# Kernel tuning notes

Hardware: AMD Instinct MI355X
Metric: run time of the kernel (lower is better)

The kernel has to match this reference:

```python
import jax, jax.numpy as jnp
import numpy as np

BETA = 0.25


def setup_inputs() -> dict:
    key = jax.random.key(0)
    k1, k2 = jax.random.split(key)
    inputs = jax.random.normal(k1, (32, 4096, 64), dtype=jnp.float32)
    # VarianceScaling(uniform) ~ small-magnitude init; plain normal scaled works for a numeric reference
    codebook = jax.random.normal(k2, (1024, 64), dtype=jnp.float32) * (1.0 / np.sqrt(64.0))
    return {"inputs": inputs, "codebook": codebook}


def reference(inputs, codebook):
    D = codebook.shape[-1]
    flat = jnp.reshape(inputs, (-1, D))                      # [N, D]
    flat_sqr = jnp.sum(flat ** 2, axis=-1, keepdims=True)    # [N, 1]
    code_sqr = jnp.sum(codebook ** 2, axis=-1)[None, :]      # [1, K]
    # full pairwise squared distances [N, K]
    distances = flat_sqr - 2.0 * (flat @ codebook.T) + code_sqr
    encoding_indices = jnp.reshape(jnp.argmin(distances, axis=-1), inputs.shape[:-1])
    quantize = codebook[encoding_indices]                    # gather -> [..., D]
    encoding_loss = jnp.mean((jax.lax.stop_gradient(inputs) - quantize) ** 2)
    commit_loss = jnp.mean((inputs - jax.lax.stop_gradient(quantize)) ** 2)
    loss = encoding_loss + BETA * commit_loss
    # straight-through estimator
    z_q = inputs + jax.lax.stop_gradient(quantize - inputs)
    return loss, z_q, encoding_indices
```

## Files before the change

kernel.cpp:

```cpp
#include <hip/hip_runtime.h>

#define N_ROWS 131072
#define D 64
#define K_CODES 1024

typedef _Float16 f16x8 __attribute__((ext_vector_type(8)));
typedef float    f32x4 __attribute__((ext_vector_type(4)));

#define MFMA16(a, b, c) __builtin_amdgcn_mfma_f32_16x16x32_f16((a), (b), (c), 0, 0, 0)

__global__ __launch_bounds__(256)
void prep_kernel(const float* __restrict__ CB, _Float16* __restrict__ CBf,
                 float* __restrict__ csqr, float* __restrict__ loss) {
    const int b = blockIdx.x, t = threadIdx.x;
    if (b < 64) {
        const int unit = b * 256 + t;
        const int tile = unit >> 8;
        const int f    = (unit >> 6) & 3;
        const int lane = unit & 63;
        const int quad = lane >> 4, lrow = lane & 15;
        const int code = tile * 16 + lrow;
        const int k0   = (f & 1) * 32 + quad * 8;
        const float* src = CB + (size_t)code * D + k0;
        float4 v0 = *(const float4*)(src);
        float4 v1 = *(const float4*)(src + 4);
        float xs[8] = {v0.x, v0.y, v0.z, v0.w, v1.x, v1.y, v1.z, v1.w};
        f16x8 o;
#pragma unroll
        for (int j = 0; j < 8; ++j) {
            float sv = -2.0f * xs[j];
            _Float16 h = (_Float16)sv;
            o[j] = (f < 2) ? h : (_Float16)(sv - (float)h);
        }
        *(f16x8*)(CBf + (size_t)unit * 8) = o;
    } else {
        if (t == 0) *loss = 0.0f;
        for (int k = t; k < K_CODES; k += 256) {
            const float4* p = (const float4*)(CB + (size_t)k * D);
            float s = 0.0f;
#pragma unroll
            for (int i = 0; i < 16; ++i) {
                float4 v = p[i];
                s += v.x * v.x + v.y * v.y + v.z * v.z + v.w * v.w;
            }
            csqr[k] = s;
        }
    }
}

__device__ __forceinline__ void gload_lds16(const void* g, void* l) {
    __builtin_amdgcn_global_load_lds(
        (const __attribute__((address_space(1))) void*)g,
        (__attribute__((address_space(3))) void*)l,
        16, 0, 0);
}

__global__ __launch_bounds__(512, 8)
void argmin_kernel(const float* __restrict__ X,
                   const _Float16* __restrict__ CBf,
                   const float* __restrict__ csqr,
                   const float* __restrict__ CB,
                   float* __restrict__ out) {
    __shared__ _Float16 Bring[2][4][2048];
    __shared__ float LsC[K_CODES];
    __shared__ int   ivfin[128];
    __shared__ float lsum[8];

    const int t    = threadIdx.x;
    const int wave = t >> 6;
    const int lane = t & 63;
    const int quad = lane >> 4;
    const int lrow = lane & 15;
    const int R0   = blockIdx.x * 128;
    const int Rw   = R0 + wave * 16;

#define STAGE(g_, buf_)                                                       \
    do {                                                                      \
        _Pragma("unroll")                                                     \
        for (int i_ = 0; i_ < 2; ++i_) {                                      \
            const int u_ = i_ * 512 + t;                                      \
            const f16x8* gp_ =                                                \
                (const f16x8*)CBf + (size_t)((g_) * 1024 + u_);               \
            gload_lds16((const void*)gp_,                                     \
                        (void*)((char*)&Bring[buf_][0][0] + (size_t)u_ * 16));\
        }                                                                     \
    } while (0)

    STAGE(0, 0);

    if (t < 256) ((float4*)LsC)[t] = ((const float4*)csqr)[t];

    f16x8 Ah[2], Al[2];
    float xsq = 0.0f;
    {
        const float* xr = X + (size_t)(Rw + lrow) * D;
#pragma unroll
        for (int ks = 0; ks < 2; ++ks) {
            const int k0 = ks * 32 + quad * 8;
            float4 v0 = *(const float4*)(xr + k0);
            float4 v1 = *(const float4*)(xr + k0 + 4);
            float xs[8] = {v0.x, v0.y, v0.z, v0.w, v1.x, v1.y, v1.z, v1.w};
            f16x8 h, l;
#pragma unroll
            for (int j = 0; j < 8; ++j) {
                xsq += xs[j] * xs[j];
                _Float16 hh = (_Float16)xs[j];
                h[j] = hh;
                l[j] = (_Float16)(xs[j] - (float)hh);
            }
            Ah[ks] = h;
            Al[ks] = l;
        }
    }

    float bestd[4];
    int   besti[4];
#pragma unroll
    for (int r = 0; r < 4; ++r) { bestd[r] = 3.0e38f; besti[r] = 0; }

    __syncthreads();

    for (int g = 0; g < 16; ++g) {
        if (g < 15) {
            STAGE(g + 1, (g + 1) & 1);
            asm volatile("s_waitcnt vmcnt(2)" ::: "memory");
        } else {
            asm volatile("s_waitcnt vmcnt(0)" ::: "memory");
        }
        __builtin_amdgcn_s_barrier();
        __builtin_amdgcn_sched_barrier(0);
        const _Float16* Bb = &Bring[g & 1][0][0];
#pragma unroll
        for (int i = 0; i < 4; ++i) {
            const f16x8* Bt = (const f16x8*)(Bb + i * 2048) + lane;
            f16x8 b0 = Bt[0], b1 = Bt[64], b2 = Bt[128], b3 = Bt[192];
            const int   c  = (g * 4 + i) * 16 + lrow;
            const float cs = LsC[c];
            f32x4 acc = {cs, cs, cs, cs};
            acc = MFMA16(Ah[0], b0, acc);
            acc = MFMA16(Ah[1], b1, acc);
            acc = MFMA16(Al[0], b0, acc);
            acc = MFMA16(Al[1], b1, acc);
            acc = MFMA16(Ah[0], b2, acc);
            acc = MFMA16(Ah[1], b3, acc);
#pragma unroll
            for (int r = 0; r < 4; ++r) {
                bool lt = acc[r] < bestd[r];
                bestd[r] = lt ? acc[r] : bestd[r];
                besti[r] = lt ? c : besti[r];
            }
        }
        __builtin_amdgcn_sched_barrier(0);
        __builtin_amdgcn_s_barrier();
    }

    float dvsum = 0.0f;
#pragma unroll
    for (int r = 0; r < 4; ++r) {
        float dv = bestd[r];
        int   iv = besti[r];
#pragma unroll
        for (int m = 1; m < 16; m <<= 1) {
            float od = __shfl_xor(dv, m, 64);
            int   oi = __shfl_xor(iv, m, 64);
            if (od < dv || (od == dv && oi < iv)) { dv = od; iv = oi; }
        }
        if (lrow == 0) {
            const int rl = wave * 16 + quad * 4 + r;
            ivfin[rl] = iv;
            out[1 + (size_t)N_ROWS * D + R0 + rl] = (float)iv;
            dvsum += dv;
        }
    }

    {
        float s = xsq + dvsum;
#pragma unroll
        for (int m = 1; m < 64; m <<= 1) s += __shfl_xor(s, m, 64);
        if (lane == 0) lsum[wave] = s;
    }
    __syncthreads();

    const float scale = 1.25f / (float)((size_t)N_ROWS * D);
    if (t == 0) {
        float L = 0.0f;
#pragma unroll
        for (int w = 0; w < 8; ++w) L += lsum[w];
        atomicAdd(out, L * scale);
    }

    float* p = out + 1 + (size_t)R0 * D;
#pragma unroll
    for (int i = 0; i < 4; ++i) {
        int q = i * 512 + t;
        int j = 4 * q + 3;
        if (q < 2047) {
            float v[4];
#pragma unroll
            for (int e = 0; e < 4; ++e) {
                int jj = j + e;
                v[e] = CB[(size_t)ivfin[jj >> 6] * D + (jj & 63)];
            }
            *(float4*)(p + j) = make_float4(v[0], v[1], v[2], v[3]);
        } else if (q == 2047) {
            p[8191] = CB[(size_t)ivfin[127] * D + 63];
        }
    }
    if (t == 0) {
        const float* c0 = CB + (size_t)ivfin[0] * D;
        p[0] = c0[0];
        p[1] = c0[1];
        p[2] = c0[2];
    }
}

extern "C" void kernel_launch(void* const* d_in, const int* in_sizes, int n_in,
                              void* d_out, int out_size, void* d_ws,
                              size_t ws_size, hipStream_t stream) {
    const float* X  = (const float*)d_in[0];
    const float* CB = (const float*)d_in[1];

    float*    csqr = (float*)d_ws;
    _Float16* CBf  = (_Float16*)((char*)d_ws + 4096);

    hipLaunchKernelGGL(prep_kernel, dim3(65), dim3(256), 0, stream,
                       CB, CBf, csqr, (float*)d_out);
    hipLaunchKernelGGL(argmin_kernel, dim3(N_ROWS / 128), dim3(512), 0, stream,
                       X, CBf, csqr, CB, (float*)d_out);
}
```

Baseline: 149.2 us.

## Halve argmin block size and prefetch code norms from global per stage

The argmin kernel now runs 256-thread blocks over 64 rows, with each codebook stage holding 2 tiles instead of 4, and the grid size doubles. The codebook-norm LDS table is removed. Each lane instead loads its code norm with inline global_load_dword, prefetched one stage ahead and kept in registers that alternate through a manually unrolled two-stage loop. This is meant to raise occupancy and cut LDS use and the initial barrier. The cost is twice as many barriers per block, since there are more stages, and more total codebook staging traffic across the larger grid.

```diff
diff --git a/kernel.cpp b/kernel.cpp
--- a/kernel.cpp
+++ b/kernel.cpp
@@ -55,40 +55,92 @@
         16, 0, 0);
 }
 
-__global__ __launch_bounds__(512, 8)
+__global__ __launch_bounds__(256, 8)
 void argmin_kernel(const float* __restrict__ X,
                    const _Float16* __restrict__ CBf,
                    const float* __restrict__ csqr,
                    const float* __restrict__ CB,
                    float* __restrict__ out) {
-    __shared__ _Float16 Bring[2][4][2048];
-    __shared__ float LsC[K_CODES];
-    __shared__ int   ivfin[128];
-    __shared__ float lsum[8];
+    __shared__ _Float16 Bring[2][2][2048];
+    __shared__ int   ivfin[64];
+    __shared__ float lsum[4];
 
     const int t    = threadIdx.x;
     const int wave = t >> 6;
     const int lane = t & 63;
     const int quad = lane >> 4;
     const int lrow = lane & 15;
-    const int R0   = blockIdx.x * 128;
+    const int R0   = blockIdx.x * 64;
     const int Rw   = R0 + wave * 16;
 
 #define STAGE(g_, buf_)                                                       \
     do {                                                                      \
         _Pragma("unroll")                                                     \
         for (int i_ = 0; i_ < 2; ++i_) {                                      \
-            const int u_ = i_ * 512 + t;                                      \
+            const int u_ = i_ * 256 + t;                                      \
             const f16x8* gp_ =                                                \
-                (const f16x8*)CBf + (size_t)((g_) * 1024 + u_);               \
+                (const f16x8*)CBf + (size_t)((g_) * 512 + u_);                \
             gload_lds16((const void*)gp_,                                     \
                         (void*)((char*)&Bring[buf_][0][0] + (size_t)u_ * 16));\
         }                                                                     \
     } while (0)
 
+#define CSLOAD(dst_, g_, i_)                                                  \
+    do {                                                                      \
+        const float* a_ = csp + ((g_) * 2 + (i_)) * 16;                       \
+        asm volatile("global_load_dword %0, %1, off"                          \
+                     : "=&v"(dst_) : "v"(a_));                                \
+    } while (0)
+
+#define WAIT4(c0_, c1_)                                                       \
+    asm volatile("s_waitcnt vmcnt(4)" : "+v"(c0_), "+v"(c1_) :: "memory")
+#define WAIT0(c0_, c1_)                                                       \
+    asm volatile("s_waitcnt vmcnt(0)" : "+v"(c0_), "+v"(c1_) :: "memory")
+
+#define TILECOMP(g_, i_, cs_)                                                 \
+    do {                                                                      \
+        const f16x8* Bt_ = (const f16x8*)&Bring[(g_) & 1][i_][0] + lane;      \
+        f16x8 b0 = Bt_[0], b1 = Bt_[64], b2 = Bt_[128], b3 = Bt_[192];        \
+        const int c_ = ((g_) * 2 + (i_)) * 16 + lrow;                         \
+        f32x4 acc = {cs_, cs_, cs_, cs_};                                     \
+        acc = MFMA16(Ah[0], b0, acc);                                         \
+        acc = MFMA16(Ah[1], b1, acc);                                         \
+        acc = MFMA16(Al[0], b0, acc);                                         \
+        acc = MFMA16(Al[1], b1, acc);                                         \
+        acc = MFMA16(Ah[0], b2, acc);                                         \
+        acc = MFMA16(Ah[1], b3, acc);                                         \
+        _Pragma("unroll")                                                     \
+        for (int r = 0; r < 4; ++r) {                                         \
+            bool lt = acc[r] < bestd[r];                                      \
+            bestd[r] = lt ? acc[r] : bestd[r];                                \
+            besti[r] = lt ? c_ : besti[r];                                    \
+        }                                                                     \
+    } while (0)
+
+#define BODY(g_, cur0_, cur1_, nxt0_, nxt1_, LAST_)                           \
+    do {                                                                      \
+        if (!(LAST_)) {                                                       \
+            CSLOAD(nxt0_, (g_) + 1, 0);                                       \
+            CSLOAD(nxt1_, (g_) + 1, 1);                                       \
+            STAGE((g_) + 1, ((g_) + 1) & 1);                                  \
+            WAIT4(cur0_, cur1_);                                              \
+        } else {                                                              \
+            WAIT0(cur0_, cur1_);                                              \
+        }                                                                     \
+        __builtin_amdgcn_s_barrier();                                         \
+        __builtin_amdgcn_sched_barrier(0);                                    \
+        TILECOMP(g_, 0, cur0_);                                               \
+        TILECOMP(g_, 1, cur1_);                                               \
+        __builtin_amdgcn_sched_barrier(0);                                    \
+        __builtin_amdgcn_s_barrier();                                         \
+    } while (0)
+
+    const float* csp = csqr + lrow;
+
+    float csA0, csA1, csB0, csB1;
+    CSLOAD(csA0, 0, 0);
+    CSLOAD(csA1, 0, 1);
     STAGE(0, 0);
-
-    if (t < 256) ((float4*)LsC)[t] = ((const float4*)csqr)[t];
 
     f16x8 Ah[2], Al[2];
     float xsq = 0.0f;
@@ -118,41 +170,12 @@
 #pragma unroll
     for (int r = 0; r < 4; ++r) { bestd[r] = 3.0e38f; besti[r] = 0; }
 
-    __syncthreads();
-
-    for (int g = 0; g < 16; ++g) {
-        if (g < 15) {
-            STAGE(g + 1, (g + 1) & 1);
-            asm volatile("s_waitcnt vmcnt(2)" ::: "memory");
-        } else {
-            asm volatile("s_waitcnt vmcnt(0)" ::: "memory");
-        }
-        __builtin_amdgcn_s_barrier();
-        __builtin_amdgcn_sched_barrier(0);
-        const _Float16* Bb = &Bring[g & 1][0][0];
-#pragma unroll
-        for (int i = 0; i < 4; ++i) {
-            const f16x8* Bt = (const f16x8*)(Bb + i * 2048) + lane;
-            f16x8 b0 = Bt[0], b1 = Bt[64], b2 = Bt[128], b3 = Bt[192];
-            const int   c  = (g * 4 + i) * 16 + lrow;
-            const float cs = LsC[c];
-            f32x4 acc = {cs, cs, cs, cs};
-            acc = MFMA16(Ah[0], b0, acc);
-            acc = MFMA16(Ah[1], b1, acc);
-            acc = MFMA16(Al[0], b0, acc);
-            acc = MFMA16(Al[1], b1, acc);
-            acc = MFMA16(Ah[0], b2, acc);
-            acc = MFMA16(Ah[1], b3, acc);
-#pragma unroll
-            for (int r = 0; r < 4; ++r) {
-                bool lt = acc[r] < bestd[r];
-                bestd[r] = lt ? acc[r] : bestd[r];
-                besti[r] = lt ? c : besti[r];
-            }
-        }
-        __builtin_amdgcn_sched_barrier(0);
-        __builtin_amdgcn_s_barrier();
-    }
+    for (int g2 = 0; g2 < 30; g2 += 2) {
+        BODY(g2,     csA0, csA1, csB0, csB1, false);
+        BODY(g2 + 1, csB0, csB1, csA0, csA1, false);
+    }
+    BODY(30, csA0, csA1, csB0, csB1, false);
+    BODY(31, csB0, csB1, csA0, csA1, true);
 
     float dvsum = 0.0f;
 #pragma unroll
@@ -182,19 +205,15 @@
     __syncthreads();
 
     const float scale = 1.25f / (float)((size_t)N_ROWS * D);
-    if (t == 0) {
-        float L = 0.0f;
-#pragma unroll
-        for (int w = 0; w < 8; ++w) L += lsum[w];
-        atomicAdd(out, L * scale);
-    }
+    if (t == 0)
+        atomicAdd(out, (lsum[0] + lsum[1] + lsum[2] + lsum[3]) * scale);
 
     float* p = out + 1 + (size_t)R0 * D;
 #pragma unroll
     for (int i = 0; i < 4; ++i) {
-        int q = i * 512 + t;
+        int q = i * 256 + t;
         int j = 4 * q + 3;
-        if (q < 2047) {
+        if (q < 1023) {
             float v[4];
 #pragma unroll
             for (int e = 0; e < 4; ++e) {
@@ -202,8 +221,8 @@
                 v[e] = CB[(size_t)ivfin[jj >> 6] * D + (jj & 63)];
             }
             *(float4*)(p + j) = make_float4(v[0], v[1], v[2], v[3]);
-        } else if (q == 2047) {
-            p[8191] = CB[(size_t)ivfin[127] * D + 63];
+        } else if (q == 1023) {
+            p[4095] = CB[(size_t)ivfin[63] * D + 63];
         }
     }
     if (t == 0) {
@@ -225,6 +244,6 @@
 
     hipLaunchKernelGGL(prep_kernel, dim3(65), dim3(256), 0, stream,
                        CB, CBf, csqr, (float*)d_out);
-    hipLaunchKernelGGL(argmin_kernel, dim3(N_ROWS / 128), dim3(512), 0, stream,
+    hipLaunchKernelGGL(argmin_kernel, dim3(N_ROWS / 64), dim3(256), 0, stream,
                        X, CBf, csqr, CB, (float*)d_out);
 }
```

Measured after the change: 157.1 us. +5.3%, slower.
